# Kernel tuning notes

Measured on AMD Instinct MI355X. Metric: run time of the kernel, lower is better.

## Reference

```python
import jax, jax.numpy as jnp
import numpy as np

N_Q, N_K = 4096, 32768
D_IN_Q, D_IN_V = 1024, 1024
D_QK, D_V = 512, 512
MASK_VAL = -1000.0


def setup_inputs() -> dict:
    key = jax.random.key(0)
    ks = jax.random.split(key, 9)
    X1 = jax.random.normal(ks[0], (N_Q, D_IN_Q), dtype=jnp.float32)
    X2 = jax.random.normal(ks[1], (N_K, D_IN_V), dtype=jnp.float32)
    row_map = jax.random.randint(ks[2], (N_K,), 0, N_Q, dtype=jnp.int32)
    # Linear params (stored as (in, out) for x @ W + b), xavier-ish scale
    def lin(k, din, dout):
        s = jnp.sqrt(6.0 / (din + dout)).astype(jnp.float32)
        return jax.random.uniform(k, (din, dout), jnp.float32, -s, s)
    Wq = lin(ks[3], D_IN_Q, D_QK); bq = jnp.zeros((D_QK,), jnp.float32)
    Wk = lin(ks[4], D_IN_V, D_QK); bk = jnp.zeros((D_QK,), jnp.float32)
    Wv = lin(ks[5], D_IN_V, D_V); bv = jnp.zeros((D_V,), jnp.float32)
    return {"X1": X1, "X2": X2, "Wq": Wq, "bq": bq, "Wk": Wk, "bk": bk,
            "Wv": Wv, "bv": bv, "row_map": row_map}


def reference(X1, X2, Wq, bq, Wk, bk, Wv, bv, row_map):
    n_q = X1.shape[0]
    n_k = X2.shape[0]
    Q = X1 @ Wq + bq                      # (n_q, d_qk)
    K = X2 @ Wk + bk                      # (n_k, d_qk)
    V = X2 @ Wv + bv                      # (n_k, d_v)
    scale = 1.0 / jnp.sqrt(jnp.float32(Q.shape[1]))
    S = (Q @ K.T) * scale                 # (n_q, n_k)
    cols = jnp.arange(n_k)
    # Keep only entries (row_map[j], j); everything else set to -1000 (as in torch)
    S_masked = jnp.full_like(S, MASK_VAL).at[row_map, cols].set(S[row_map, cols])
    W = jax.nn.softmax(S_masked, axis=1)  # (n_q, n_k)
    C = W @ V                             # (n_q, d_v)
    # Queries with no related keys get zero rows (torch skips them entirely)
    counts = jax.ops.segment_sum(jnp.ones((n_k,), jnp.float32), row_map,
                                 num_segments=n_q)
    return jnp.where(counts[:, None] > 0, C, jnp.zeros_like(C))
```

## Files before the change

kernel.cpp:

```cpp
#include <hip/hip_runtime.h>

typedef unsigned short bhalf;
typedef __bf16 bf16x8 __attribute__((ext_vector_type(8)));
typedef float f32x4 __attribute__((ext_vector_type(4)));

#define NQ 4096
#define NK 32768
#define DIN 1024
#define DQK 512
#define SCALE 0.044194173824159216f

__device__ __forceinline__ unsigned f2bf(float f) {
  union { float f; unsigned u; } c; c.f = f;
  unsigned u = c.u;
  return (u + 0x7fffu + ((u >> 16) & 1u)) >> 16;
}

__global__ __launch_bounds__(256) void prep_kernel(
    const float* __restrict__ X1, const float* __restrict__ Wq,
    const float* __restrict__ Wk, const float* __restrict__ Wv,
    const float* __restrict__ bq, const float* __restrict__ bk,
    const int* __restrict__ rm,
    bhalf* __restrict__ X1b, bhalf* __restrict__ Wq_b, bhalf* __restrict__ Wk_b,
    bhalf* __restrict__ WvT, float* __restrict__ g_s, float* __restrict__ h,
    float* __restrict__ scal, int* __restrict__ cnt) {
  __shared__ float tile[32][33];
  const int b = blockIdx.x;
  const int tid = threadIdx.x;
  if (b < 5120) {
    const float* in; bhalf* out; int idx;
    if (b < 4096)      { in = X1; out = X1b; idx = b * 256 + tid; }
    else if (b < 4608) { in = Wq; out = Wq_b; idx = (b - 4096) * 256 + tid; }
    else               { in = Wk; out = Wk_b; idx = (b - 4608) * 256 + tid; }
    float4 v = ((const float4*)in)[idx];
    uint2 o;
    o.x = f2bf(v.x) | (f2bf(v.y) << 16);
    o.y = f2bf(v.z) | (f2bf(v.w) << 16);
    ((uint2*)out)[idx] = o;
  } else if (b < 5632) {
    const int bb = b - 5120;
    const int bx = bb & 15, by = bb >> 4;
    const int tx = tid & 31, ty = tid >> 5;
    const int x = bx * 32 + tx;
#pragma unroll
    for (int yy = 0; yy < 32; yy += 8)
      tile[ty + yy][tx] = Wv[(size_t)(by * 32 + ty + yy) * 512 + x];
    __syncthreads();
    const int k = by * 32 + tx;
#pragma unroll
    for (int yy = 0; yy < 32; yy += 8)
      WvT[(size_t)(bx * 32 + ty + yy) * 1024 + k] = (bhalf)f2bf(tile[tx][ty + yy]);
  } else if (b < 6145) {
    const int w = (b - 5632) * 4 + (tid >> 6);
    const int lane = tid & 63;
    if (w >= 2049) return;
    const float* row; const float* vec;
    if (w < 1024)      { row = Wk + (size_t)w * 512; vec = bq; }
    else if (w < 2048) { row = Wq + (size_t)(w - 1024) * 512; vec = bk; }
    else               { row = bq; vec = bk; }
    float s = 0.f;
#pragma unroll
    for (int t = 0; t < 2; t++) {
      float4 a = *(const float4*)(row + t * 256 + lane * 4);
      float4 bb2 = *(const float4*)(vec + t * 256 + lane * 4);
      s += a.x * bb2.x + a.y * bb2.y + a.z * bb2.z + a.w * bb2.w;
    }
#pragma unroll
    for (int d = 32; d; d >>= 1) s += __shfl_xor(s, d);
    if (lane == 0) {
      if (w < 1024) g_s[w] = s * SCALE;
      else if (w < 2048) h[w - 1024] = s;
      else scal[0] = s;
    }
  } else {
    const int j = (b - 6145) * 256 + tid;
    atomicAdd(&cnt[rm[j]], 1);
  }
}

template <int MODE, int MI>
__global__ __launch_bounds__(256) void gemm_core(
    const bhalf* __restrict__ A, const bhalf* __restrict__ Bt,
    const float* __restrict__ bias, const int* __restrict__ cnt,
    void* __restrict__ Cout, int M, int N, int K, int nnt) {
  __shared__ __align__(16) bhalf As[MI * 32 * 64];
  __shared__ __align__(16) bhalf Bs[128 * 64];
  const int bid = blockIdx.x;
  const int mt = bid / nnt, nt = bid % nnt;
  const int bmb = mt * (MI * 32), bnb = nt * 128;

  const int tid = threadIdx.x;
  const int lane = tid & 63;
  const int wv = tid >> 6;
  const int wm = (wv & 1) * (MI * 16);
  const int wn = (wv >> 1) * 64;
  const int quad = lane >> 4;
  const int l15 = lane & 15;

  f32x4 acc[MI][4];
#pragma unroll
  for (int i = 0; i < MI; i++)
#pragma unroll
    for (int j = 0; j < 4; j++)
#pragma unroll
      for (int r = 0; r < 4; r++) acc[i][j][r] = 0.0f;

  const int srow = lane >> 3;
  const int scol = (lane & 7) ^ srow;

  for (int kb = 0; kb < K; kb += 64) {
    const size_t goff = (size_t)kb + (size_t)scol * 8;
#pragma unroll
    for (int r = 0; r < MI; r++) {
      const int chunk = wv * MI + r;
      const int row = chunk * 8 + srow;
      __builtin_amdgcn_global_load_lds(
          (__attribute__((address_space(1))) unsigned int*)(A + (size_t)(bmb + row) * K + goff),
          (__attribute__((address_space(3))) unsigned int*)(As + chunk * 512), 16, 0, 0);
    }
#pragma unroll
    for (int r = 0; r < 4; r++) {
      const int chunk = wv * 4 + r;
      const int row = chunk * 8 + srow;
      __builtin_amdgcn_global_load_lds(
          (__attribute__((address_space(1))) unsigned int*)(Bt + (size_t)(bnb + row) * K + goff),
          (__attribute__((address_space(3))) unsigned int*)(Bs + chunk * 512), 16, 0, 0);
    }
    __syncthreads();
#pragma unroll
    for (int ks = 0; ks < 2; ks++) {
      const int su = ((ks * 4 + quad) ^ (lane & 7)) * 8;
      bf16x8 af[MI], bfr[4];
#pragma unroll
      for (int i = 0; i < MI; i++)
        af[i] = *(const bf16x8*)(As + (wm + i * 16 + l15) * 64 + su);
#pragma unroll
      for (int j = 0; j < 4; j++)
        bfr[j] = *(const bf16x8*)(Bs + (wn + j * 16 + l15) * 64 + su);
#pragma unroll
      for (int i = 0; i < MI; i++)
#pragma unroll
        for (int j = 0; j < 4; j++)
          acc[i][j] = __builtin_amdgcn_mfma_f32_16x16x32_bf16(af[i], bfr[j], acc[i][j], 0, 0, 0);
    }
    __syncthreads();
  }
#pragma unroll
  for (int j = 0; j < 4; j++) {
    const int col = bnb + wn + j * 16 + l15;
    const float bs = (MODE >= 1) ? bias[col] : 0.0f;
#pragma unroll
    for (int i = 0; i < MI; i++) {
#pragma unroll
      for (int r = 0; r < 4; r++) {
        const int row = bmb + wm + i * 16 + quad * 4 + r;
        const float v = acc[i][j][r];
        if (MODE == 0) {
          ((bhalf*)Cout)[(size_t)row * N + col] = (bhalf)f2bf(v * SCALE);
        } else if (MODE == 1) {
          ((float*)Cout)[(size_t)row * N + col] = v + bs;
        } else {
          ((float*)Cout)[(size_t)row * N + col] = (cnt[row] > 0) ? (v + bs) : 0.0f;
        }
      }
    }
  }
}

__global__ __launch_bounds__(1024) void scan_kernel(const int* __restrict__ cnt,
                                                    int* __restrict__ off,
                                                    int* __restrict__ cur) {
  const int t = threadIdx.x;
  int4 v = ((const int4*)cnt)[t];
  const int sum = v.x + v.y + v.z + v.w;
  const int lane = t & 63, w = t >> 6;
  int x = sum;
#pragma unroll
  for (int d = 1; d < 64; d <<= 1) {
    int y = __shfl_up(x, d);
    if (lane >= d) x += y;
  }
  __shared__ int wsum[16];
  if (lane == 63) wsum[w] = x;
  __syncthreads();
  if (t == 0) {
    int a = 0;
    for (int i = 0; i < 16; i++) { int tv = wsum[i]; wsum[i] = a; a += tv; }
  }
  __syncthreads();
  const int excl = x - sum + wsum[w];
  int4 o; o.x = excl; o.y = o.x + v.x; o.z = o.y + v.y; o.w = o.z + v.z;
  ((int4*)off)[t] = o;
  ((int4*)cur)[t] = o;
}

__global__ void scatter_kernel(const int* __restrict__ rm, int* __restrict__ cur,
                               int* __restrict__ keylist) {
  const int j = blockIdx.x * 256 + threadIdx.x;
  const int p = atomicAdd(&cur[rm[j]], 1);
  keylist[p] = j;
}

__global__ __launch_bounds__(256) void scorewsum_kernel(
    const float* __restrict__ P, const float* __restrict__ X1,
    const float* __restrict__ X2, const float* __restrict__ h,
    const float* __restrict__ scal, const int* __restrict__ off,
    const int* __restrict__ cnt, const int* __restrict__ keylist,
    bhalf* __restrict__ Ub) {
  const int wv = threadIdx.x >> 6;
  const int i = blockIdx.x * 4 + wv;
  const int lane = threadIdx.x & 63;
  const int c = cnt[i], base = off[i];
  const float* Prow = P + (size_t)i * 1024;
  float4 p[4];
#pragma unroll
  for (int t = 0; t < 4; t++) p[t] = *(const float4*)(Prow + t * 256 + lane * 4);
  const float* x1r = X1 + (size_t)i * 1024;
  float s0 = 0.f;
#pragma unroll
  for (int t = 0; t < 4; t++) {
    float4 a = *(const float4*)(x1r + t * 256 + lane * 4);
    float4 b = *(const float4*)(h + t * 256 + lane * 4);
    s0 += a.x * b.x + a.y * b.y + a.z * b.z + a.w * b.w;
  }
#pragma unroll
  for (int d = 32; d; d >>= 1) s0 += __shfl_xor(s0, d);
  const float e_i = (s0 + scal[0]) * SCALE;

  float sumw = 0.f;
  float4 u[4] = {};
  for (int pp = 0; pp < c; pp++) {
    const int j = keylist[base + pp];
    const float* xr = X2 + (size_t)j * 1024;
    float4 x[4];
#pragma unroll
    for (int t = 0; t < 4; t++) x[t] = *(const float4*)(xr + t * 256 + lane * 4);
    float s = 0.f;
#pragma unroll
    for (int t = 0; t < 4; t++)
      s += p[t].x * x[t].x + p[t].y * x[t].y + p[t].z * x[t].z + p[t].w * x[t].w;
#pragma unroll
    for (int d = 32; d; d >>= 1) s += __shfl_xor(s, d);
    const float w = __expf(s + e_i);
    sumw += w;
#pragma unroll
    for (int t = 0; t < 4; t++) {
      u[t].x += w * x[t].x; u[t].y += w * x[t].y;
      u[t].z += w * x[t].z; u[t].w += w * x[t].w;
    }
  }
  const float inv = (c > 0) ? 1.f / sumw : 0.f;
  bhalf* urow = Ub + (size_t)i * 1024;
#pragma unroll
  for (int t = 0; t < 4; t++) {
    uint2 o;
    o.x = f2bf(u[t].x * inv) | (f2bf(u[t].y * inv) << 16);
    o.y = f2bf(u[t].z * inv) | (f2bf(u[t].w * inv) << 16);
    *(uint2*)(urow + t * 256 + lane * 4) = o;
  }
}

extern "C" void kernel_launch(void* const* d_in, const int* in_sizes, int n_in,
                              void* d_out, int out_size, void* d_ws, size_t ws_size,
                              hipStream_t stream) {
  const float* X1 = (const float*)d_in[0];
  const float* X2 = (const float*)d_in[1];
  const float* Wq = (const float*)d_in[2];
  const float* bq = (const float*)d_in[3];
  const float* Wk = (const float*)d_in[4];
  const float* bk = (const float*)d_in[5];
  const float* Wv = (const float*)d_in[6];
  const float* bv = (const float*)d_in[7];
  const int* row_map = (const int*)d_in[8];
  float* out = (float*)d_out;

  char* p = (char*)d_ws;
  bhalf* X1b  = (bhalf*)p; p += (size_t)NQ * DIN * 2;
  bhalf* Wq_b = (bhalf*)p; p += (size_t)DIN * DQK * 2;
  bhalf* Wk_b = (bhalf*)p; p += (size_t)DIN * DQK * 2;
  bhalf* WvT  = (bhalf*)p; p += (size_t)DQK * DIN * 2;
  bhalf* Bt2  = (bhalf*)p; p += (size_t)DIN * DIN * 2;
  float* Pbuf = (float*)p; p += (size_t)NQ * DIN * 4;
  bhalf* Ub   = (bhalf*)p; p += (size_t)NQ * DIN * 2;
  float* g_s  = (float*)p; p += DIN * 4;
  float* h    = (float*)p; p += DIN * 4;
  float* scal = (float*)p; p += 256;
  int* cnt    = (int*)p;   p += NQ * 4;
  int* off    = (int*)p;   p += NQ * 4;
  int* cur    = (int*)p;   p += NQ * 4;
  int* keylist = (int*)p;  p += NK * 4;

  hipMemsetAsync(cnt, 0, (size_t)NQ * 4, stream);

  prep_kernel<<<6273, 256, 0, stream>>>(X1, Wq, Wk, Wv, bq, bk, row_map,
                                        X1b, Wq_b, Wk_b, WvT, g_s, h, scal, cnt);
  scan_kernel<<<1, 1024, 0, stream>>>(cnt, off, cur);
  scatter_kernel<<<NK / 256, 256, 0, stream>>>(row_map, cur, keylist);

  gemm_core<0, 2><<<128, 256, 0, stream>>>(Wk_b, Wq_b, nullptr, nullptr, Bt2, 1024, 1024, 512, 8);
  gemm_core<1, 4><<<256, 256, 0, stream>>>(X1b, Bt2, g_s, nullptr, Pbuf, 4096, 1024, 1024, 8);

  scorewsum_kernel<<<NQ / 4, 256, 0, stream>>>(Pbuf, X1, X2, h, scal, off, cnt, keylist, Ub);

  gemm_core<2, 2><<<256, 256, 0, stream>>>(Ub, WvT, bv, cnt, out, 4096, 512, 1024, 4);
}
```

Before: 297.2 us.

## Drop per-row softmax constant and store projected query matrix in bf16

```diff
diff --git a/kernel.cpp b/kernel.cpp
--- a/kernel.cpp
+++ b/kernel.cpp
@@ -15,15 +15,19 @@
   unsigned u = c.u;
   return (u + 0x7fffu + ((u >> 16) & 1u)) >> 16;
 }
+__device__ __forceinline__ float bf_lo(unsigned u) {
+  union { unsigned u; float f; } c; c.u = u << 16; return c.f;
+}
+__device__ __forceinline__ float bf_hi(unsigned u) {
+  union { unsigned u; float f; } c; c.u = u & 0xffff0000u; return c.f;
+}
 
 __global__ __launch_bounds__(256) void prep_kernel(
     const float* __restrict__ X1, const float* __restrict__ Wq,
     const float* __restrict__ Wk, const float* __restrict__ Wv,
-    const float* __restrict__ bq, const float* __restrict__ bk,
-    const int* __restrict__ rm,
+    const float* __restrict__ bq, const int* __restrict__ rm,
     bhalf* __restrict__ X1b, bhalf* __restrict__ Wq_b, bhalf* __restrict__ Wk_b,
-    bhalf* __restrict__ WvT, float* __restrict__ g_s, float* __restrict__ h,
-    float* __restrict__ scal, int* __restrict__ cnt) {
+    bhalf* __restrict__ WvT, float* __restrict__ g_s, int* __restrict__ cnt) {
   __shared__ float tile[32][33];
   const int b = blockIdx.x;
   const int tid = threadIdx.x;
@@ -50,30 +54,22 @@
 #pragma unroll
     for (int yy = 0; yy < 32; yy += 8)
       WvT[(size_t)(bx * 32 + ty + yy) * 1024 + k] = (bhalf)f2bf(tile[tx][ty + yy]);
-  } else if (b < 6145) {
+  } else if (b < 5888) {
     const int w = (b - 5632) * 4 + (tid >> 6);
     const int lane = tid & 63;
-    if (w >= 2049) return;
-    const float* row; const float* vec;
-    if (w < 1024)      { row = Wk + (size_t)w * 512; vec = bq; }
-    else if (w < 2048) { row = Wq + (size_t)(w - 1024) * 512; vec = bk; }
-    else               { row = bq; vec = bk; }
+    const float* row = Wk + (size_t)w * 512;
     float s = 0.f;
 #pragma unroll
     for (int t = 0; t < 2; t++) {
       float4 a = *(const float4*)(row + t * 256 + lane * 4);
-      float4 bb2 = *(const float4*)(vec + t * 256 + lane * 4);
+      float4 bb2 = *(const float4*)(bq + t * 256 + lane * 4);
       s += a.x * bb2.x + a.y * bb2.y + a.z * bb2.z + a.w * bb2.w;
     }
 #pragma unroll
     for (int d = 32; d; d >>= 1) s += __shfl_xor(s, d);
-    if (lane == 0) {
-      if (w < 1024) g_s[w] = s * SCALE;
-      else if (w < 2048) h[w - 1024] = s;
-      else scal[0] = s;
-    }
+    if (lane == 0) g_s[w] = s * SCALE;
   } else {
-    const int j = (b - 6145) * 256 + tid;
+    const int j = (b - 5888) * 256 + tid;
     atomicAdd(&cnt[rm[j]], 1);
   }
 }
@@ -158,7 +154,7 @@
         if (MODE == 0) {
           ((bhalf*)Cout)[(size_t)row * N + col] = (bhalf)f2bf(v * SCALE);
         } else if (MODE == 1) {
-          ((float*)Cout)[(size_t)row * N + col] = v + bs;
+          ((bhalf*)Cout)[(size_t)row * N + col] = (bhalf)f2bf(v + bs);
         } else {
           ((float*)Cout)[(size_t)row * N + col] = (cnt[row] > 0) ? (v + bs) : 0.0f;
         }
@@ -202,30 +198,25 @@
 }
 
 __global__ __launch_bounds__(256) void scorewsum_kernel(
-    const float* __restrict__ P, const float* __restrict__ X1,
-    const float* __restrict__ X2, const float* __restrict__ h,
-    const float* __restrict__ scal, const int* __restrict__ off,
-    const int* __restrict__ cnt, const int* __restrict__ keylist,
-    bhalf* __restrict__ Ub) {
+    const bhalf* __restrict__ P, const float* __restrict__ X2,
+    const int* __restrict__ off, const int* __restrict__ cnt,
+    const int* __restrict__ keylist, bhalf* __restrict__ Ub) {
   const int wv = threadIdx.x >> 6;
   const int i = blockIdx.x * 4 + wv;
   const int lane = threadIdx.x & 63;
   const int c = cnt[i], base = off[i];
-  const float* Prow = P + (size_t)i * 1024;
-  float4 p[4];
-#pragma unroll
-  for (int t = 0; t < 4; t++) p[t] = *(const float4*)(Prow + t * 256 + lane * 4);
-  const float* x1r = X1 + (size_t)i * 1024;
-  float s0 = 0.f;
-#pragma unroll
-  for (int t = 0; t < 4; t++) {
-    float4 a = *(const float4*)(x1r + t * 256 + lane * 4);
-    float4 b = *(const float4*)(h + t * 256 + lane * 4);
-    s0 += a.x * b.x + a.y * b.y + a.z * b.z + a.w * b.w;
-  }
-#pragma unroll
-  for (int d = 32; d; d >>= 1) s0 += __shfl_xor(s0, d);
-  const float e_i = (s0 + scal[0]) * SCALE;
+  const bhalf* Prow = P + (size_t)i * 1024;
+  uint4 pb[2];
+#pragma unroll
+  for (int t = 0; t < 2; t++) pb[t] = *(const uint4*)(Prow + t * 512 + lane * 8);
+  float pf[16];
+#pragma unroll
+  for (int t = 0; t < 2; t++) {
+    pf[t * 8 + 0] = bf_lo(pb[t].x); pf[t * 8 + 1] = bf_hi(pb[t].x);
+    pf[t * 8 + 2] = bf_lo(pb[t].y); pf[t * 8 + 3] = bf_hi(pb[t].y);
+    pf[t * 8 + 4] = bf_lo(pb[t].z); pf[t * 8 + 5] = bf_hi(pb[t].z);
+    pf[t * 8 + 6] = bf_lo(pb[t].w); pf[t * 8 + 7] = bf_hi(pb[t].w);
+  }
 
   float sumw = 0.f;
   float4 u[4] = {};
@@ -234,14 +225,18 @@
     const float* xr = X2 + (size_t)j * 1024;
     float4 x[4];
 #pragma unroll
-    for (int t = 0; t < 4; t++) x[t] = *(const float4*)(xr + t * 256 + lane * 4);
+    for (int t = 0; t < 2; t++) {
+      x[t * 2]     = *(const float4*)(xr + t * 512 + lane * 8);
+      x[t * 2 + 1] = *(const float4*)(xr + t * 512 + lane * 8 + 4);
+    }
     float s = 0.f;
 #pragma unroll
     for (int t = 0; t < 4; t++)
-      s += p[t].x * x[t].x + p[t].y * x[t].y + p[t].z * x[t].z + p[t].w * x[t].w;
+      s += pf[t * 4 + 0] * x[t].x + pf[t * 4 + 1] * x[t].y
+         + pf[t * 4 + 2] * x[t].z + pf[t * 4 + 3] * x[t].w;
 #pragma unroll
     for (int d = 32; d; d >>= 1) s += __shfl_xor(s, d);
-    const float w = __expf(s + e_i);
+    const float w = __expf(s);
     sumw += w;
 #pragma unroll
     for (int t = 0; t < 4; t++) {
@@ -252,11 +247,13 @@
   const float inv = (c > 0) ? 1.f / sumw : 0.f;
   bhalf* urow = Ub + (size_t)i * 1024;
 #pragma unroll
-  for (int t = 0; t < 4; t++) {
-    uint2 o;
-    o.x = f2bf(u[t].x * inv) | (f2bf(u[t].y * inv) << 16);
-    o.y = f2bf(u[t].z * inv) | (f2bf(u[t].w * inv) << 16);
-    *(uint2*)(urow + t * 256 + lane * 4) = o;
+  for (int t = 0; t < 2; t++) {
+    uint4 o;
+    o.x = f2bf(u[t * 2].x * inv) | (f2bf(u[t * 2].y * inv) << 16);
+    o.y = f2bf(u[t * 2].z * inv) | (f2bf(u[t * 2].w * inv) << 16);
+    o.z = f2bf(u[t * 2 + 1].x * inv) | (f2bf(u[t * 2 + 1].y * inv) << 16);
+    o.w = f2bf(u[t * 2 + 1].z * inv) | (f2bf(u[t * 2 + 1].w * inv) << 16);
+    *(uint4*)(urow + t * 512 + lane * 8) = o;
   }
 }
 
@@ -268,9 +265,8 @@
   const float* Wq = (const float*)d_in[2];
   const float* bq = (const float*)d_in[3];
   const float* Wk = (const float*)d_in[4];
-  const float* bk = (const float*)d_in[5];
+  const float* bv = (const float*)d_in[7];
   const float* Wv = (const float*)d_in[6];
-  const float* bv = (const float*)d_in[7];
   const int* row_map = (const int*)d_in[8];
   float* out = (float*)d_out;
 
@@ -280,11 +276,9 @@
   bhalf* Wk_b = (bhalf*)p; p += (size_t)DIN * DQK * 2;
   bhalf* WvT  = (bhalf*)p; p += (size_t)DQK * DIN * 2;
   bhalf* Bt2  = (bhalf*)p; p += (size_t)DIN * DIN * 2;
-  float* Pbuf = (float*)p; p += (size_t)NQ * DIN * 4;
+  bhalf* Pbuf = (bhalf*)p; p += (size_t)NQ * DIN * 2;
   bhalf* Ub   = (bhalf*)p; p += (size_t)NQ * DIN * 2;
   float* g_s  = (float*)p; p += DIN * 4;
-  float* h    = (float*)p; p += DIN * 4;
-  float* scal = (float*)p; p += 256;
   int* cnt    = (int*)p;   p += NQ * 4;
   int* off    = (int*)p;   p += NQ * 4;
   int* cur    = (int*)p;   p += NQ * 4;
@@ -292,15 +286,15 @@
 
   hipMemsetAsync(cnt, 0, (size_t)NQ * 4, stream);
 
-  prep_kernel<<<6273, 256, 0, stream>>>(X1, Wq, Wk, Wv, bq, bk, row_map,
-                                        X1b, Wq_b, Wk_b, WvT, g_s, h, scal, cnt);
+  prep_kernel<<<6016, 256, 0, stream>>>(X1, Wq, Wk, Wv, bq, row_map,
+                                        X1b, Wq_b, Wk_b, WvT, g_s, cnt);
   scan_kernel<<<1, 1024, 0, stream>>>(cnt, off, cur);
   scatter_kernel<<<NK / 256, 256, 0, stream>>>(row_map, cur, keylist);
 
   gemm_core<0, 2><<<128, 256, 0, stream>>>(Wk_b, Wq_b, nullptr, nullptr, Bt2, 1024, 1024, 512, 8);
   gemm_core<1, 4><<<256, 256, 0, stream>>>(X1b, Bt2, g_s, nullptr, Pbuf, 4096, 1024, 1024, 8);
 
-  scorewsum_kernel<<<NQ / 4, 256, 0, stream>>>(Pbuf, X1, X2, h, scal, off, cnt, keylist, Ub);
+  scorewsum_kernel<<<NQ / 4, 256, 0, stream>>>(Pbuf, X2, off, cnt, keylist, Ub);
 
   gemm_core<2, 2><<<256, 256, 0, stream>>>(Ub, WvT, bv, cnt, out, 4096, 512, 1024, 4);
 }
```

Result: no change. 294.0 us (-1.1%).
